# Kernel tuning notes

Measured on AMD Instinct MI355X. Metric: run time of the kernel, lower is better.

## Reference

```python
import jax, jax.numpy as jnp
import numpy as np

# ---- fixed architecture hyperparameters (match init_kwargs) ----
B, S = 4, 1024
L, H, DM, DF = 4, 8, 512, 2048
DH = DM // H          # 64 head dim (= 2*R after gated SPE filter)
NS = 5                # num_sines
R = 32                # num_realizations
M = 2 * DH            # favor_feature_dims = 128 (split as +/- of 64 projections)
LN_EPS = 1e-5
ATT_EPS = 1e-6


def layernorm(x, g, b):
    mu = x.mean(-1, keepdims=True)
    var = ((x - mu) ** 2).mean(-1, keepdims=True)
    return (x - mu) * jax.lax.rsqrt(var + LN_EPS) * g + b


def sine_spe(freqs, offsets, gains, noise, seq_len):
    """SineSPE positional code. freqs/offsets/gains: (H,DH,NS); noise: (H,DH,2NS,R).
    Returns qbar, kbar of shape (S,H,DH,R)."""
    pos = jnp.arange(seq_len, dtype=freqs.dtype)
    f = jax.nn.sigmoid(freqs)[:, :, None, :] / 2.0                       # (H,DH,1,NS)
    ph_q = 2.0 * jnp.pi * f * pos[None, None, :, None] + offsets[:, :, None, :]
    ph_k = 2.0 * jnp.pi * f * pos[None, None, :, None]
    om_q = jnp.stack([jnp.cos(ph_q), jnp.sin(ph_q)], -1).reshape(H, DH, seq_len, 2 * NS)
    om_k = jnp.stack([jnp.cos(ph_k), jnp.sin(ph_k)], -1).reshape(H, DH, seq_len, 2 * NS)
    g = jax.nn.softplus(gains)
    g = jnp.stack([g, g], -1).reshape(H, DH, 2 * NS)                      # upsample gains
    z = noise * g[..., None] / jnp.sqrt(jnp.asarray(2.0 * NS, freqs.dtype))
    qbar = jnp.einsum('hdsk,hdkr->shdr', om_q, z)
    kbar = jnp.einsum('hdsk,hdkr->shdr', om_k, z)
    scale = (R * DH) ** 0.25
    return qbar / scale, kbar / scale


def spe_filter(q, k, qbar, kbar, gate, gnoise):
    """Gated SPE filter. q,k: (B,S,H,DH); qbar/kbar: (S,H,DH,R); gate: (H,DH); gnoise: (H,DH,R).
    Returns qhat, khat of shape (B,S,H,2R)."""
    g = jax.nn.sigmoid(gate)[..., None]                                   # (H,DH,1)
    gn = gnoise / (DH * R) ** 0.25
    seq_len = qbar.shape[0]
    bias = jnp.broadcast_to(jnp.sqrt(g) * gn, (seq_len, H, DH, R))
    qb = jnp.concatenate([jnp.sqrt(1.0 - g) * qbar, bias], -1)            # (S,H,DH,2R)
    kb = jnp.concatenate([jnp.sqrt(1.0 - g) * kbar, bias], -1)
    qhat = jnp.einsum('bshd,shdr->bshr', q, qb)
    khat = jnp.einsum('bshd,shdr->bshr', k, kb)
    return qhat, khat


def favor(x, omega):
    """FAVOR+ softmax feature map. x: (B,S,H,DH); omega: (DH, M//2) -> (B,S,H,M)."""
    x = x * (DH ** -0.25)                                                 # sqrt(softmax_temp), temp=1/sqrt(DH)
    half_norm = 0.5 * jnp.sum(x * x, -1, keepdims=True)
    u = jnp.einsum('bshe,em->bshm', x, omega)
    phi = jnp.concatenate([jnp.exp(u - half_norm), jnp.exp(-u - half_norm)], -1)
    return phi / jnp.sqrt(jnp.asarray(M, x.dtype))


def causal_linear_attention(Q, K, V):
    """Causal linear (kernelized) attention via lax.scan. Q,K: (B,S,H,M); V: (B,S,H,DH)."""
    Bv = Q.shape[0]

    def step(carry, qkv):
        Skv, sk = carry
        q, k, v = qkv                                                     # (B,H,M),(B,H,M),(B,H,DH)
        Skv = Skv + jnp.einsum('bhm,bhd->bhmd', k, v)
        sk = sk + k
        num = jnp.einsum('bhm,bhmd->bhd', q, Skv)
        den = jnp.einsum('bhm,bhm->bh', q, sk) + ATT_EPS
        return (Skv, sk), num / den[..., None]

    init = (jnp.zeros((Bv, H, M, DH), Q.dtype), jnp.zeros((Bv, H, M), Q.dtype))
    xs = tuple(jnp.moveaxis(t, 1, 0) for t in (Q, K, V))
    _, out = jax.lax.scan(step, init, xs)
    return jnp.moveaxis(out, 0, 1)                                        # (B,S,H,DH)


def setup_inputs() -> dict:
    key = jax.random.key(0)
    ks = jax.random.split(key, 14)

    def rn(k, shape, scale=1.0):
        return jax.random.normal(k, shape, dtype=jnp.float32) * scale

    return {
        'x': rn(ks[0], (B, S, DM)),
        'Wq': rn(ks[1], (L, DM, DM), 0.02), 'bq': jnp.zeros((L, DM), jnp.float32),
        'Wk': rn(ks[2], (L, DM, DM), 0.02), 'bk': jnp.zeros((L, DM), jnp.float32),
        'Wv': rn(ks[3], (L, DM, DM), 0.02), 'bv': jnp.zeros((L, DM), jnp.float32),
        'Wo': rn(ks[4], (L, DM, DM), 0.02), 'bo': jnp.zeros((L, DM), jnp.float32),
        'W1': rn(ks[5], (L, DM, DF), 0.02), 'b1': jnp.zeros((L, DF), jnp.float32),
        'W2': rn(ks[6], (L, DF, DM), 0.02), 'b2': jnp.zeros((L, DM), jnp.float32),
        'ln1_g': jnp.ones((L, DM), jnp.float32), 'ln1_b': jnp.zeros((L, DM), jnp.float32),
        'ln2_g': jnp.ones((L, DM), jnp.float32), 'ln2_b': jnp.zeros((L, DM), jnp.float32),
        'spe_freqs': rn(ks[7], (L, H, DH, NS)),
        'spe_offsets': rn(ks[8], (L, H, DH, NS)),
        'spe_gains': rn(ks[9], (L, H, DH, NS)),
        'spe_noise': rn(ks[10], (L, H, DH, 2 * NS, R)),
        'gate': rn(ks[11], (L, H, DH)),
        'gate_noise': rn(ks[12], (L, H, DH, R)),
        'favor_omega': rn(ks[13], (L, DH, M // 2)),
    }


def reference(x, Wq, bq, Wk, bk, Wv, bv, Wo, bo, W1, b1, W2, b2,
              ln1_g, ln1_b, ln2_g, ln2_b,
              spe_freqs, spe_offsets, spe_gains, spe_noise, gate, gate_noise, favor_omega):
    Bv, Sv, _ = x.shape
    out = x
    for l in range(L):
        qbar, kbar = sine_spe(spe_freqs[l], spe_offsets[l], spe_gains[l], spe_noise[l], Sv)
        q = (out @ Wq[l] + bq[l]).reshape(Bv, Sv, H, DH)
        k = (out @ Wk[l] + bk[l]).reshape(Bv, Sv, H, DH)
        v = (out @ Wv[l] + bv[l]).reshape(Bv, Sv, H, DH)
        qh, kh = spe_filter(q, k, qbar, kbar, gate[l], gate_noise[l])
        Qf = favor(qh, favor_omega[l])
        Kf = favor(kh, favor_omega[l])
        att = causal_linear_attention(Qf, Kf, v).reshape(Bv, Sv, DM)
        att = att @ Wo[l] + bo[l]
        h = layernorm(out + att, ln1_g[l], ln1_b[l])
        y = jax.nn.relu(h @ W1[l] + b1[l]) @ W2[l] + b2[l]
        out = layernorm(h + y, ln2_g[l], ln2_b[l])
    return out
```

## Files before the change

kernel.cpp:

```cpp
#include <hip/hip_runtime.h>
#include <math.h>

#define BB 4
#define SS 1024
#define LL 4
#define HH 8
#define DM 512
#define DF 2048
#define DH 64
#define NS 5
#define RR 32
#define MM 128
#define NC 16
#define CHK 64
#define QKV_N 1536

#define INV_SQRT10   0.316227766016838f
#define INV_SCALE    0.148650889375340f
#define TEMP_SCALE   0.353553390593274f
#define INV_SQRT_M   0.088388347648318f
#define TWO_PI       6.283185307179586f
#define PI_F         3.141592653589793f

typedef __attribute__((ext_vector_type(8))) short bf16x8;
typedef __attribute__((ext_vector_type(4))) float f32x4;

__device__ __forceinline__ unsigned short f2bf(float f) {
  union { float f; unsigned int u; } v; v.f = f;
  unsigned int r = v.u + 0x7FFFu + ((v.u >> 16) & 1u);
  return (unsigned short)(r >> 16);
}

__device__ __forceinline__ float bf2f(unsigned short u) {
  union { unsigned int u; float f; } v; v.u = (unsigned int)u << 16;
  return v.f;
}

__device__ __forceinline__ void gld_lds16(const unsigned short* g, unsigned short* l) {
  __builtin_amdgcn_global_load_lds((const __attribute__((address_space(1))) void*)g,
                                   (__attribute__((address_space(3))) void*)l,
                                   16, 0, 0);
}

template<int RELU, int OUT_BF, int SPLITK>
__global__ __launch_bounds__(256)
void gemm_mfma_n64(const unsigned short* __restrict__ A, const unsigned short* __restrict__ Bt,
                   const float* __restrict__ bias, float* __restrict__ Cf,
                   unsigned short* __restrict__ Cbf, int M, int N, int K)
{
  __shared__ unsigned short As[128 * 32];
  __shared__ unsigned short Bs[64 * 32];
  const int tid  = threadIdx.x;
  const int w    = tid >> 6;
  const int lane = tid & 63;
  const int row0 = blockIdx.y * 128;
  const int col0 = blockIdx.x * 64;
  const int kz   = (SPLITK > 1) ? blockIdx.z : 0;
  const int Ks   = K / SPLITK;
  const int kbeg = kz * Ks;
  const int wr = (w >> 1) * 64;
  const int wc = (w & 1) * 32;
  const int c0 = w * 2, c1 = w * 2 + 1;
  const int m0 = c0 * 16 + (lane >> 2);
  const int m1 = c1 * 16 + (lane >> 2);
  const int mb = w * 16 + (lane >> 2);
  const int kA = (lane & 3) * 8;

  f32x4 acc[4][2] = {};

  for (int k0 = kbeg; k0 < kbeg + Ks; k0 += 32) {
    gld_lds16(&A [(size_t)(row0 + m0) * K + k0 + kA], &As[c0 * 512]);
    gld_lds16(&A [(size_t)(row0 + m1) * K + k0 + kA], &As[c1 * 512]);
    gld_lds16(&Bt[(size_t)(col0 + mb) * K + k0 + kA], &Bs[w * 512]);
    __syncthreads();
    const int rA = wr + (lane & 15);
    const int rB = wc + (lane & 15);
    const int kk = (lane >> 4) * 8;
    bf16x8 af[4], bfr[2];
#pragma unroll
    for (int i = 0; i < 4; ++i)
      af[i]  = *reinterpret_cast<const bf16x8*>(&As[(rA + i * 16) * 32 + kk]);
#pragma unroll
    for (int i = 0; i < 2; ++i)
      bfr[i] = *reinterpret_cast<const bf16x8*>(&Bs[(rB + i * 16) * 32 + kk]);
#pragma unroll
    for (int mi = 0; mi < 4; ++mi)
#pragma unroll
      for (int ni = 0; ni < 2; ++ni)
        acc[mi][ni] = __builtin_amdgcn_mfma_f32_16x16x32_bf16(af[mi], bfr[ni], acc[mi][ni], 0, 0, 0);
    __syncthreads();
  }
  const int cr = (lane >> 4) * 4;
  const int cc = lane & 15;
  float* Cfo = Cf ? (Cf + (size_t)kz * M * N) : Cf;
  unsigned short* Cbo = Cbf ? (Cbf + (size_t)kz * M * N) : Cbf;
#pragma unroll
  for (int mi = 0; mi < 4; ++mi) {
#pragma unroll
    for (int ni = 0; ni < 2; ++ni) {
      const int col = col0 + wc + ni * 16 + cc;
      const float bv = (kz == 0) ? bias[col] : 0.f;
#pragma unroll
      for (int r = 0; r < 4; ++r) {
        const int row = row0 + wr + mi * 16 + cr + r;
        float v = acc[mi][ni][r] + bv;
        if (RELU) v = fmaxf(v, 0.f);
        if (OUT_BF) Cbo[(size_t)row * N + col] = f2bf(v);
        else        Cfo[(size_t)row * N + col] = v;
      }
    }
  }
}

#define PR_T0   4096
#define PR_W1   8192
#define PR_W2   12288
#define PR_OM   12304
#define PR_PB   12328
#define PR_SP   15224
#define PR_CV   17272

__global__ __launch_bounds__(256)
void prep_all(const float* __restrict__ x,
              const float* __restrict__ Wq, const float* __restrict__ Wk,
              const float* __restrict__ Wv, const float* __restrict__ Wo,
              const float* __restrict__ W1, const float* __restrict__ W2,
              const float* __restrict__ omega,
              const float* __restrict__ bq, const float* __restrict__ bk,
              const float* __restrict__ bv,
              const float* __restrict__ gains, const float* __restrict__ noise,
              const float* __restrict__ gate, const float* __restrict__ gnoise,
              const float* __restrict__ offsets, const float* __restrict__ freqs,
              unsigned short* __restrict__ curbf,
              unsigned short* __restrict__ Wqkvt, unsigned short* __restrict__ Wot,
              unsigned short* __restrict__ W1t, unsigned short* __restrict__ W2t,
              unsigned short* __restrict__ omgT,
              float* __restrict__ bqkv,
              unsigned short* __restrict__ zpb, unsigned short* __restrict__ wbb,
              float2* __restrict__ offcs, float* __restrict__ omg)
{
  const int bid = blockIdx.x;
  const int tid = threadIdx.x;

  if (bid < PR_OM) {
    const float* W; unsigned short* Wt; int K, N, bx, by;
    if (bid < PR_T0) {
      const int mat = bid >> 10;
      const int local = bid & 1023;
      bx = local & 15; by = (local >> 4) & 15;
      const int l = local >> 8;
      K = DM; N = DM;
      if (mat == 0)      { W = Wq + (size_t)l * DM * DM; Wt = Wqkvt + (size_t)l * QKV_N * DM; }
      else if (mat == 1) { W = Wk + (size_t)l * DM * DM; Wt = Wqkvt + (size_t)l * QKV_N * DM + (size_t)512 * DM; }
      else if (mat == 2) { W = Wv + (size_t)l * DM * DM; Wt = Wqkvt + (size_t)l * QKV_N * DM + (size_t)1024 * DM; }
      else               { W = Wo + (size_t)l * DM * DM; Wt = Wot + (size_t)l * DM * DM; }
    } else if (bid < PR_W1) {
      const int local = bid - PR_T0;
      bx = local & 63; by = (local >> 6) & 15;
      const int l = local >> 10;
      K = DM; N = DF;
      W = W1 + (size_t)l * DM * DF; Wt = W1t + (size_t)l * DF * DM;
    } else if (bid < PR_W2) {
      const int local = bid - PR_W1;
      bx = local & 15; by = (local >> 4) & 63;
      const int l = local >> 10;
      K = DF; N = DM;
      W = W2 + (size_t)l * DF * DM; Wt = W2t + (size_t)l * DM * DF;
    } else {
      const int local = bid - PR_W2;
      bx = local & 1; by = (local >> 1) & 1;
      const int l = local >> 2;
      K = DH; N = MM / 2;
      W = omega + (size_t)l * DH * (MM / 2); Wt = omgT + (size_t)l * 4096;
    }
    __shared__ float tile[32][33];
    const int k0 = by * 32, n0 = bx * 32;
    const int tx = tid & 31, ty = tid >> 5;
#pragma unroll
    for (int j = 0; j < 4; ++j)
      tile[ty + 8 * j][tx] = W[(size_t)(k0 + ty + 8 * j) * N + n0 + tx];
    __syncthreads();
#pragma unroll
    for (int j = 0; j < 4; ++j)
      Wt[(size_t)(n0 + ty + 8 * j) * K + k0 + tx] = f2bf(tile[tx][ty + 8 * j]);
  } else if (bid < PR_PB) {
    const int local = bid - PR_OM;
    const int l = local / 6;
    const int i = (local % 6) * 256 + tid;
    if (i < QKV_N)
      bqkv[l * QKV_N + i] = (i < 512) ? bq[l * DM + i] : (i < 1024) ? bk[l * DM + i - 512]
                                                                    : bv[l * DM + i - 1024];
  } else if (bid < PR_SP) {
    const int i = (bid - PR_PB) * 256 + tid;
    const int NZ = LL * HH * RR * 10 * DH;
    const int NW = LL * HH * RR * DH;
    const int NO = LL * HH * DH * NS;
    if (i < NZ) {
      const int d = i & 63;
      int j = i >> 6;
      const int k = j % 10; j /= 10;
      const int r = j & 31; j >>= 5;
      const int h = j & 7;  const int l = j >> 3;
      const int lhd = (l * HH + h) * DH + d;
      const float ga = gains[lhd * NS + (k >> 1)];
      const float sp = (ga > 20.f) ? ga : log1pf(__expf(ga));
      const float gg = 1.f / (1.f + __expf(-gate[lhd]));
      const float c1 = sqrtf(fmaxf(1.f - gg, 0.f));
      const float nz = noise[((size_t)lhd * 10 + k) * 32 + r];
      zpb[i] = f2bf(nz * sp * c1 * (INV_SQRT10 * INV_SCALE * TEMP_SCALE));
    } else if (i < NZ + NW) {
      int j = i - NZ;
      const int d = j & 63; j >>= 6;
      const int r = j & 31; j >>= 5;
      const int h = j & 7;  const int l = j >> 3;
      const int lhd = (l * HH + h) * DH + d;
      const float gg = 1.f / (1.f + __expf(-gate[lhd]));
      wbb[i - NZ] = f2bf(sqrtf(gg) * gnoise[(size_t)lhd * 32 + r] * (INV_SCALE * TEMP_SCALE));
    } else if (i < NZ + NW + NO) {
      const int j = i - NZ - NW;
      float sn, cn;
      __sincosf(offsets[j], &sn, &cn);
      offcs[j] = make_float2(cn, sn);
    } else if (i < NZ + NW + 2 * NO) {
      const int j = i - NZ - NW - NO;
      omg[j] = PI_F / (1.f + __expf(-freqs[j]));
    }
  } else {
    const int i = (bid - PR_SP) * 256 + tid;
    const int n4 = BB * SS * DM / 4;
    if (i < n4) {
      const float4 v = reinterpret_cast<const float4*>(x)[i];
      ushort4 o;
      o.x = f2bf(v.x); o.y = f2bf(v.y); o.z = f2bf(v.z); o.w = f2bf(v.w);
      reinterpret_cast<ushort4*>(curbf)[i] = o;
    }
  }
}

__global__ __launch_bounds__(256)
void spe_xhat(const float* __restrict__ omg, const float2* __restrict__ offcs,
              const unsigned short* __restrict__ zpb, const unsigned short* __restrict__ wbb,
              const unsigned short* __restrict__ qkvb, const unsigned short* __restrict__ omgT,
              unsigned short* __restrict__ QfKfB)
{
  const int s = blockIdx.x;
  const int h = blockIdx.y;
  const int t = threadIdx.x;
  const int w = t >> 6;
  const int lane = t & 63;
  __shared__ float omqT[10][64];
  __shared__ float omkT[10][64];
  __shared__ unsigned short qbT[64 * 64];
  __shared__ unsigned short kbT[64 * 64];
  __shared__ unsigned short rQ[16 * 64];
  __shared__ unsigned short rK[16 * 64];
  __shared__ float hqp[4][8];
  __shared__ float hnl[8];

  for (int e = t; e < DH * NS; e += 256) {
    const int d = e / NS, ns = e - d * NS;
    const float om = omg[(h * DH + d) * NS + ns];
    float sn, cn;
    __sincosf(om * (float)s, &sn, &cn);
    const float2 oc = offcs[(h * DH + d) * NS + ns];
    omkT[2 * ns][d]     = cn;
    omkT[2 * ns + 1][d] = sn;
    omqT[2 * ns][d]     = cn * oc.x - sn * oc.y;
    omqT[2 * ns + 1][d] = sn * oc.x + cn * oc.y;
  }
  if (t < 64) {
    const int isK = t >> 5;
    const int b = (t >> 3) & 3;
    const int j = t & 7;
    const unsigned short* src = qkvb + ((size_t)b * SS + s) * QKV_N + isK * 512 + h * DH + j * 8;
    unsigned short* dst = (isK ? rK : rQ) + b * 64 + ((j ^ b) << 3);
    *reinterpret_cast<bf16x8*>(dst) = *reinterpret_cast<const bf16x8*>(src);
  } else if (t < 256) {
    const int i = t - 64;
    bf16x8 z = {};
    if (i < 96) *reinterpret_cast<bf16x8*>(&rQ[256 + i * 8]) = z;
    else        *reinterpret_cast<bf16x8*>(&rK[256 + (i - 96) * 8]) = z;
  }
  __syncthreads();
  {
    const int r = t >> 3, dg = t & 7, d0 = dg * 8;
    float accq[8] = {}, acck[8] = {};
    const unsigned short* zr = zpb + (size_t)(h * RR + r) * 10 * 64 + d0;
#pragma unroll
    for (int k = 0; k < 10; ++k) {
      const bf16x8 zv = *reinterpret_cast<const bf16x8*>(zr + (size_t)k * 64);
      const float4 oq0 = *reinterpret_cast<const float4*>(&omqT[k][d0]);
      const float4 oq1 = *reinterpret_cast<const float4*>(&omqT[k][d0 + 4]);
      const float4 ok0 = *reinterpret_cast<const float4*>(&omkT[k][d0]);
      const float4 ok1 = *reinterpret_cast<const float4*>(&omkT[k][d0 + 4]);
      float zf[8];
#pragma unroll
      for (int j = 0; j < 8; ++j) zf[j] = bf2f((unsigned short)zv[j]);
      accq[0] += zf[0] * oq0.x; accq[1] += zf[1] * oq0.y;
      accq[2] += zf[2] * oq0.z; accq[3] += zf[3] * oq0.w;
      accq[4] += zf[4] * oq1.x; accq[5] += zf[5] * oq1.y;
      accq[6] += zf[6] * oq1.z; accq[7] += zf[7] * oq1.w;
      acck[0] += zf[0] * ok0.x; acck[1] += zf[1] * ok0.y;
      acck[2] += zf[2] * ok0.z; acck[3] += zf[3] * ok0.w;
      acck[4] += zf[4] * ok1.x; acck[5] += zf[5] * ok1.y;
      acck[6] += zf[6] * ok1.z; acck[7] += zf[7] * ok1.w;
    }
    bf16x8 qv, kv;
#pragma unroll
    for (int j = 0; j < 8; ++j) {
      qv[j] = (short)f2bf(accq[j]);
      kv[j] = (short)f2bf(acck[j]);
    }
    const int sd0 = d0 ^ ((r & 7) << 3);
    *reinterpret_cast<bf16x8*>(&qbT[r * 64 + sd0]) = qv;
    *reinterpret_cast<bf16x8*>(&kbT[r * 64 + sd0]) = kv;
    const bf16x8 wv = *reinterpret_cast<const bf16x8*>(&wbb[(size_t)(h * RR + r) * 64 + d0]);
    *reinterpret_cast<bf16x8*>(&qbT[(32 + r) * 64 + sd0]) = wv;
    *reinterpret_cast<bf16x8*>(&kbT[(32 + r) * 64 + sd0]) = wv;
  }
  __syncthreads();
  f32x4 aq = {0.f, 0.f, 0.f, 0.f}, ak = {0.f, 0.f, 0.f, 0.f};
  const int arow = lane & 15;
  const int colr = w * 16 + (lane & 15);
#pragma unroll
  for (int kt = 0; kt < 2; ++kt) {
    const int g = kt * 4 + (lane >> 4);
    const bf16x8 fAq = *reinterpret_cast<const bf16x8*>(&rQ[arow * 64 + ((g ^ (arow & 7)) << 3)]);
    const bf16x8 fAk = *reinterpret_cast<const bf16x8*>(&rK[arow * 64 + ((g ^ (arow & 7)) << 3)]);
    const bf16x8 fBq = *reinterpret_cast<const bf16x8*>(&qbT[colr * 64 + ((g ^ (colr & 7)) << 3)]);
    const bf16x8 fBk = *reinterpret_cast<const bf16x8*>(&kbT[colr * 64 + ((g ^ (colr & 7)) << 3)]);
    aq = __builtin_amdgcn_mfma_f32_16x16x32_bf16(fAq, fBq, aq, 0, 0, 0);
    ak = __builtin_amdgcn_mfma_f32_16x16x32_bf16(fAk, fBk, ak, 0, 0, 0);
  }
  float rq[4], rk2[4];
#pragma unroll
  for (int r = 0; r < 4; ++r) { rq[r] = aq[r] * aq[r]; rk2[r] = ak[r] * ak[r]; }
#pragma unroll
  for (int off = 1; off < 16; off <<= 1) {
#pragma unroll
    for (int r = 0; r < 4; ++r) {
      rq[r]  += __shfl_xor(rq[r],  off, 64);
      rk2[r] += __shfl_xor(rk2[r], off, 64);
    }
  }
  if (lane == 0) {
#pragma unroll
    for (int r = 0; r < 4; ++r) { hqp[w][r] = rq[r]; hqp[w][4 + r] = rk2[r]; }
  }
  __syncthreads();

  if (t < 8) {
    const int b = t & 3;
    const int ko = (t >> 2) * 4;
    hnl[t] = 0.5f * (hqp[0][ko + b] + hqp[1][ko + b] + hqp[2][ko + b] + hqp[3][ko + b]);
  }
  if (lane < 16) {
#pragma unroll
    for (int r = 0; r < 4; ++r) {
      const int d = w * 16 + lane;
      rQ[r * 64 + (d ^ (r << 3))] = f2bf(aq[r]);
      rK[r * 64 + (d ^ (r << 3))] = f2bf(ak[r]);
    }
  }
  __syncthreads();

  f32x4 uq = {0.f, 0.f, 0.f, 0.f}, uk = {0.f, 0.f, 0.f, 0.f};
  const int ocol = w * 16 + (lane & 15);
#pragma unroll
  for (int kt = 0; kt < 2; ++kt) {
    const int g = kt * 4 + (lane >> 4);
    const bf16x8 fAq = *reinterpret_cast<const bf16x8*>(&rQ[arow * 64 + ((g ^ (arow & 7)) << 3)]);
    const bf16x8 fAk = *reinterpret_cast<const bf16x8*>(&rK[arow * 64 + ((g ^ (arow & 7)) << 3)]);
    const bf16x8 fB  = *reinterpret_cast<const bf16x8*>(&omgT[(size_t)ocol * 64 + g * 8]);
    uq = __builtin_amdgcn_mfma_f32_16x16x32_bf16(fAq, fB, uq, 0, 0, 0);
    uk = __builtin_amdgcn_mfma_f32_16x16x32_bf16(fAk, fB, uk, 0, 0, 0);
  }
  if (lane < 16) {
#pragma unroll
    for (int r = 0; r < 4; ++r) {
      const size_t rowq = ((size_t)r * SS + s) * HH + h;
      const size_t rowk = rowq + (size_t)BB * SS * HH;
      const float hq = hnl[r], hk = hnl[4 + r];
      QfKfB[rowq * MM + ocol]      = f2bf(__expf( uq[r] - hq) * INV_SQRT_M);
      QfKfB[rowq * MM + ocol + 64] = f2bf(__expf(-uq[r] - hq) * INV_SQRT_M);
      QfKfB[rowk * MM + ocol]      = f2bf(__expf( uk[r] - hk) * INV_SQRT_M);
      QfKfB[rowk * MM + ocol + 64] = f2bf(__expf(-uk[r] - hk) * INV_SQRT_M);
    }
  }
}

__global__ __launch_bounds__(256)
void attn_chunk_sums(const unsigned short* __restrict__ KfB, const unsigned short* __restrict__ qkvb,
                     unsigned short* __restrict__ SchB, float* __restrict__ kch)
{
  const int c = blockIdx.x, h = blockIdx.y, b = blockIdx.z;
  const int tid = threadIdx.x;
  const int w = tid >> 6, lane = tid & 63;
  __shared__ unsigned short KcT[128 * 64];
  __shared__ unsigned short VT[64 * 64];
  const size_t srow0 = (size_t)b * SS + c * CHK;

  for (int i = tid; i < 8192; i += 256) {
    const int m = i & 127, t = i >> 7;
    KcT[m * 64 + (t ^ ((m & 7) << 3))] = KfB[((srow0 + t) * HH + h) * MM + m];
  }
  for (int i = tid; i < 512; i += 256) {
    const int d = i & 63, oct = i >> 6;
    const unsigned short* src = qkvb + (srow0 + oct * 8) * QKV_N + 1024 + h * DH + d;
    bf16x8 v;
#pragma unroll
    for (int j = 0; j < 8; ++j) v[j] = (short)src[(size_t)j * QKV_N];
    *reinterpret_cast<bf16x8*>(&VT[d * 64 + ((oct << 3) ^ ((d & 7) << 3))]) = v;
  }
  __syncthreads();

  const int kk = (lane >> 4) * 8;
  f32x4 acc[2][4] = {};
#pragma unroll
  for (int kc = 0; kc < 2; ++kc) {
    const int k = kc * 32 + kk;
#pragma unroll
    for (int mi = 0; mi < 2; ++mi) {
      const int mA = w * 32 + mi * 16 + (lane & 15);
      const bf16x8 a = *reinterpret_cast<const bf16x8*>(&KcT[mA * 64 + (k ^ ((mA & 7) << 3))]);
#pragma unroll
      for (int ni = 0; ni < 4; ++ni) {
        const int dB = ni * 16 + (lane & 15);
        const bf16x8 bb = *reinterpret_cast<const bf16x8*>(&VT[dB * 64 + (k ^ ((dB & 7) << 3))]);
        acc[mi][ni] = __builtin_amdgcn_mfma_f32_16x16x32_bf16(a, bb, acc[mi][ni], 0, 0, 0);
      }
    }
  }
  const size_t base = (((size_t)b * HH + h) * NC + c);
  unsigned short* So = SchB + base * (MM * DH);
  const int cr = (lane >> 4) * 4, cc = lane & 15;
#pragma unroll
  for (int mi = 0; mi < 2; ++mi)
#pragma unroll
    for (int ni = 0; ni < 4; ++ni)
#pragma unroll
      for (int r = 0; r < 4; ++r)
        So[(size_t)(w * 32 + mi * 16 + cr + r) * DH + ni * 16 + cc] = f2bf(acc[mi][ni][r]);
  {
    const int m = tid >> 1, half = tid & 1;
    float ks = 0.f;
#pragma unroll
    for (int j = 0; j < 32; ++j) {
      const int t2 = half * 32 + j;
      ks += bf2f(KcT[m * 64 + (t2 ^ ((m & 7) << 3))]);
    }
    ks += __shfl_xor(ks, 1, 64);
    if (half == 0) kch[base * MM + m] = ks;
  }
}

__global__ __launch_bounds__(256)
void attn_scan(unsigned short* __restrict__ SchB, float* __restrict__ kch)
{
  const int bh = blockIdx.x, part = blockIdx.y;
  const int t = threadIdx.x;
  unsigned short* base = SchB + (size_t)bh * NC * (MM * DH);
  {
    const int e0 = part * 1024 + t * 4;
    float run0 = 0.f, run1 = 0.f, run2 = 0.f, run3 = 0.f;
#pragma unroll
    for (int c = 0; c < NC; ++c) {
      ushort4* p = reinterpret_cast<ushort4*>(&base[(size_t)c * (MM * DH) + e0]);
      const ushort4 v = *p;
      ushort4 o;
      o.x = f2bf(run0); o.y = f2bf(run1); o.z = f2bf(run2); o.w = f2bf(run3);
      *p = o;
      run0 += bf2f(v.x); run1 += bf2f(v.y); run2 += bf2f(v.z); run3 += bf2f(v.w);
    }
  }
  if (part == 0 && t < MM) {
    float* kb2 = kch + (size_t)bh * NC * MM;
    float run = 0.f;
#pragma unroll
    for (int c = 0; c < NC; ++c) {
      const float v = kb2[c * MM + t];
      kb2[c * MM + t] = run;
      run += v;
    }
  }
}

__global__ __launch_bounds__(256)
void attn_out(const unsigned short* __restrict__ QfKfB, const unsigned short* __restrict__ qkvb,
              const unsigned short* __restrict__ SchB, const float* __restrict__ kch,
              unsigned short* __restrict__ att)
{
  const int c = blockIdx.x, h = blockIdx.y, b = blockIdx.z;
  const int tid = threadIdx.x;
  const int w = tid >> 6;
  const int lane = tid & 63;
  __shared__ unsigned short Qc[64 * 128];
  __shared__ unsigned short Sb[64 * 64];
  __shared__ unsigned short KVU[12288];
  __shared__ float skp[MM];
  __shared__ float denl[64];

  unsigned short* Kc   = KVU;
  unsigned short* SpxT = KVU;
  unsigned short* VT   = KVU + 8192;

  const size_t srow0 = (size_t)b * SS + c * CHK;
  const unsigned short* Qg = QfKfB + (srow0 * HH + h) * MM;
  const unsigned short* Kg = Qg + (size_t)BB * SS * HH * MM;

  if (tid < MM) skp[tid] = kch[(((size_t)b * HH + h) * NC + c) * MM + tid];

  for (int i = tid; i < 1024; i += 256) {
    const int s2 = i >> 4, m8 = (i & 15) * 8;
    const int sw = m8 ^ ((s2 & 15) << 3);
    *reinterpret_cast<bf16x8*>(&Qc[s2 * 128 + sw]) =
        *reinterpret_cast<const bf16x8*>(&Qg[(size_t)s2 * (HH * MM) + m8]);
    *reinterpret_cast<bf16x8*>(&Kc[s2 * 128 + sw]) =
        *reinterpret_cast<const bf16x8*>(&Kg[(size_t)s2 * (HH * MM) + m8]);
  }
  for (int i = tid; i < 512; i += 256) {
    const int d = i & 63, oct = i >> 6;
    const unsigned short* src = qkvb + (srow0 + oct * 8) * QKV_N + 1024 + h * DH + d;
    bf16x8 v;
#pragma unroll
    for (int j = 0; j < 8; ++j) v[j] = (short)src[(size_t)j * QKV_N];
    *reinterpret_cast<bf16x8*>(&VT[d * 64 + ((oct << 3) ^ ((d & 7) << 3))]) = v;
  }
  __syncthreads();

  const int sA = w * 16 + (lane & 15);
  const int kk = (lane >> 4) * 8;
  f32x4 acc_s[4] = {};
#pragma unroll
  for (int kc = 0; kc < 4; ++kc) {
    const int k = kc * 32 + kk;
    const bf16x8 aq = *reinterpret_cast<const bf16x8*>(&Qc[sA * 128 + (k ^ ((sA & 15) << 3))]);
#pragma unroll
    for (int n = 0; n < 4; ++n) {
      const int tB = n * 16 + (lane & 15);
      const bf16x8 bq = *reinterpret_cast<const bf16x8*>(&Kc[tB * 128 + (k ^ ((tB & 15) << 3))]);
      acc_s[n] = __builtin_amdgcn_mfma_f32_16x16x32_bf16(aq, bq, acc_s[n], 0, 0, 0);
    }
  }
  __syncthreads();

  {
    const int g = lane >> 4;
    const int tcol = lane & 15;
    float dintra[4] = {0.f, 0.f, 0.f, 0.f};
#pragma unroll
    for (int r = 0; r < 4; ++r) {
      const int s = w * 16 + g * 4 + r;
#pragma unroll
      for (int n = 0; n < 4; ++n) {
        const int t2 = n * 16 + tcol;
        const float v = (t2 <= s) ? acc_s[n][r] : 0.f;
        dintra[r] += v;
        Sb[s * 64 + (t2 ^ ((s & 7) << 3))] = f2bf(v);
      }
    }
#pragma unroll
    for (int off = 1; off < 16; off <<= 1)
#pragma unroll
      for (int r = 0; r < 4; ++r) dintra[r] += __shfl_xor(dintra[r], off, 64);
    if (tcol == 0) {
#pragma unroll
      for (int r = 0; r < 4; ++r) denl[w * 16 + g * 4 + r] = dintra[r];
    }
  }
  {
    const unsigned short* Sp = SchB + (((size_t)b * HH + h) * NC + c) * (MM * DH);
    for (int i = tid; i < 1024; i += 256) {
      const int d = i & 63, oct = i >> 6;
      const unsigned short* src = Sp + (size_t)(oct * 8) * DH + d;
      bf16x8 v;
#pragma unroll
      for (int j = 0; j < 8; ++j) v[j] = (short)src[(size_t)j * DH];
      *reinterpret_cast<bf16x8*>(&SpxT[d * 128 + ((oct * 8) ^ ((d & 15) << 3))]) = v;
    }
  }
  __syncthreads();

  f32x4 acc_o[4] = {};
#pragma unroll
  for (int kc = 0; kc < 2; ++kc) {
    const int k = kc * 32 + kk;
    const bf16x8 as = *reinterpret_cast<const bf16x8*>(&Sb[sA * 64 + (k ^ ((sA & 7) << 3))]);
#pragma unroll
    for (int n = 0; n < 4; ++n) {
      const int dB = n * 16 + (lane & 15);
      const bf16x8 bv = *reinterpret_cast<const bf16x8*>(&VT[dB * 64 + (k ^ ((dB & 7) << 3))]);
      acc_o[n] = __builtin_amdgcn_mfma_f32_16x16x32_bf16(as, bv, acc_o[n], 0, 0, 0);
    }
  }
#pragma unroll
  for (int kc = 0; kc < 4; ++kc) {
    const int k = kc * 32 + kk;
    const bf16x8 aq = *reinterpret_cast<const bf16x8*>(&Qc[sA * 128 + (k ^ ((sA & 15) << 3))]);
#pragma unroll
    for (int n = 0; n < 4; ++n) {
      const int dB = n * 16 + (lane & 15);
      const bf16x8 bs = *reinterpret_cast<const bf16x8*>(&SpxT[dB * 128 + (k ^ ((dB & 15) << 3))]);
      acc_o[n] = __builtin_amdgcn_mfma_f32_16x16x32_bf16(aq, bs, acc_o[n], 0, 0, 0);
    }
  }
  {
    const int s2 = tid >> 2, part = tid & 3;
    float p = 0.f;
#pragma unroll
    for (int j = 0; j < 32; ++j) {
      const int m = part * 32 + j;
      p += bf2f(Qc[s2 * 128 + (m ^ ((s2 & 15) << 3))]) * skp[m];
    }
    p += __shfl_xor(p, 1, 64);
    p += __shfl_xor(p, 2, 64);
    if (part == 0) denl[s2] += p + 1e-6f;
  }
  __syncthreads();

  {
    const int g = lane >> 4;
    const int dcol = lane & 15;
#pragma unroll
    for (int r = 0; r < 4; ++r) {
      const int s = w * 16 + g * 4 + r;
      const float dinv = 1.f / denl[s];
#pragma unroll
      for (int n = 0; n < 4; ++n)
        att[(srow0 + s) * DM + h * DH + n * 16 + dcol] = f2bf(acc_o[n][r] * dinv);
    }
  }
}

template<int WBF>
__global__ __launch_bounds__(256)
void add_ln(const float* __restrict__ a, const unsigned short* __restrict__ bres, size_t sstride,
            const float* __restrict__ g, const float* __restrict__ be,
            float* __restrict__ out, unsigned short* __restrict__ outbf)
{
  const int row = blockIdx.x;
  const int t = threadIdx.x;
  const size_t base = (size_t)row * DM;
  float x0 = a[base + t]       + bf2f(bres[base + t])       + bf2f(bres[sstride + base + t]);
  float x1 = a[base + t + 256] + bf2f(bres[base + t + 256]) + bf2f(bres[sstride + base + t + 256]);
  __shared__ float red[8];
  float ssum = x0 + x1;
#pragma unroll
  for (int off = 32; off > 0; off >>= 1) ssum += __shfl_xor(ssum, off, 64);
  const int wid = t >> 6, lid = t & 63;
  if (lid == 0) red[wid] = ssum;
  __syncthreads();
  const float mu = (red[0] + red[1] + red[2] + red[3]) * (1.f / DM);
  const float d0 = x0 - mu, d1 = x1 - mu;
  float sv = d0 * d0 + d1 * d1;
#pragma unroll
  for (int off = 32; off > 0; off >>= 1) sv += __shfl_xor(sv, off, 64);
  if (lid == 0) red[4 + wid] = sv;
  __syncthreads();
  const float var = (red[4] + red[5] + red[6] + red[7]) * (1.f / DM);
  const float rs = rsqrtf(var + 1e-5f);
  const float o0 = d0 * rs * g[t]       + be[t];
  const float o1 = d1 * rs * g[t + 256] + be[t + 256];
  out[base + t]       = o0;
  out[base + t + 256] = o1;
  if (WBF) {
    outbf[base + t]       = f2bf(o0);
    outbf[base + t + 256] = f2bf(o1);
  }
}

extern "C" void kernel_launch(void* const* d_in, const int* in_sizes, int n_in,
                              void* d_out, int out_size, void* d_ws, size_t ws_size,
                              hipStream_t stream)
{
  const float* x      = (const float*)d_in[0];
  const float* Wq     = (const float*)d_in[1];
  const float* bq     = (const float*)d_in[2];
  const float* Wk     = (const float*)d_in[3];
  const float* bk     = (const float*)d_in[4];
  const float* Wv     = (const float*)d_in[5];
  const float* bv     = (const float*)d_in[6];
  const float* Wo     = (const float*)d_in[7];
  const float* bo     = (const float*)d_in[8];
  const float* W1     = (const float*)d_in[9];
  const float* b1     = (const float*)d_in[10];
  const float* W2     = (const float*)d_in[11];
  const float* b2     = (const float*)d_in[12];
  const float* ln1g   = (const float*)d_in[13];
  const float* ln1b   = (const float*)d_in[14];
  const float* ln2g   = (const float*)d_in[15];
  const float* ln2b   = (const float*)d_in[16];
  const float* freqs  = (const float*)d_in[17];
  const float* offs   = (const float*)d_in[18];
  const float* gains  = (const float*)d_in[19];
  const float* noise  = (const float*)d_in[20];
  const float* gate   = (const float*)d_in[21];
  const float* gnoise = (const float*)d_in[22];
  const float* omega  = (const float*)d_in[23];

  float* ws = (float*)d_ws;
  size_t o = 0;
  float* curf = ws + o; o += (size_t)BB * SS * DM;
  unsigned short* qkvb = (unsigned short*)(ws + o); o += (size_t)BB * SS * QKV_N / 2;
  float* Sch  = ws + o; o += (size_t)BB * HH * NC * MM * DH;
  float* kch  = ws + o; o += (size_t)BB * HH * NC * MM;
  float* bqkv = ws + o; o += (size_t)LL * QKV_N;
  float2* offcs = (float2*)(ws + o); o += (size_t)LL * HH * DH * NS * 2;
  float* omgf = ws + o; o += (size_t)LL * HH * DH * NS;
  unsigned short* zpb = (unsigned short*)(ws + o); o += (size_t)LL * HH * RR * 10 * DH / 2;
  unsigned short* QfKfB = (unsigned short*)(ws + o); o += (size_t)2 * BB * SS * HH * MM / 2;
  unsigned short* attb  = (unsigned short*)(ws + o); o += (size_t)BB * SS * DM / 2;
  unsigned short* h_bf  = (unsigned short*)(ws + o); o += (size_t)BB * SS * DM / 2;
  unsigned short* curbf = (unsigned short*)(ws + o); o += (size_t)BB * SS * DM / 2;
  unsigned short* Wqkvt = (unsigned short*)(ws + o); o += (size_t)LL * QKV_N * DM / 2;
  unsigned short* Wot   = (unsigned short*)(ws + o); o += (size_t)LL * DM * DM / 2;
  unsigned short* W1t   = (unsigned short*)(ws + o); o += (size_t)LL * DF * DM / 2;
  unsigned short* W2t   = (unsigned short*)(ws + o); o += (size_t)LL * DM * DF / 2;
  unsigned short* omgT  = (unsigned short*)(ws + o); o += (size_t)LL * 4096 / 2;
  unsigned short* wbb   = (unsigned short*)(ws + o); o += (size_t)LL * HH * RR * DH / 2;

  const size_t SLICE = (size_t)BB * SS * DM;
  unsigned short* SchB  = (unsigned short*)Sch;
  unsigned short* attpB = (unsigned short*)Sch;
  unsigned short* ybufB = (unsigned short*)Sch;
  float* hbuf = (float*)qkvb;
  unsigned short* midbf = QfKfB;
  unsigned short* KfB   = QfKfB + (size_t)BB * SS * HH * MM;

  const int MROWS = BB * SS;

  prep_all<<<PR_CV, 256, 0, stream>>>(x, Wq, Wk, Wv, Wo, W1, W2, omega,
                                      bq, bk, bv, gains, noise, gate, gnoise, offs, freqs,
                                      curbf, Wqkvt, Wot, W1t, W2t, omgT, bqkv,
                                      zpb, wbb, offcs, omgf);

  for (int l = 0; l < LL; ++l) {
    const float* in = (l == 0) ? x : curf;

    gemm_mfma_n64<0, 1, 1><<<dim3(QKV_N / 64, MROWS / 128), 256, 0, stream>>>(
        curbf, Wqkvt + (size_t)l * QKV_N * DM, bqkv + (size_t)l * QKV_N,
        (float*)nullptr, qkvb, MROWS, QKV_N, DM);

    spe_xhat<<<dim3(SS, HH), 256, 0, stream>>>(
        omgf + (size_t)l * HH * DH * NS, offcs + (size_t)l * HH * DH * NS,
        zpb + (size_t)l * HH * RR * 10 * DH, wbb + (size_t)l * HH * RR * DH,
        qkvb, omgT + (size_t)l * 4096, QfKfB);

    attn_chunk_sums<<<dim3(NC, HH, BB), 256, 0, stream>>>(KfB, qkvb, SchB, kch);
    attn_scan<<<dim3(BB * HH, 8), 256, 0, stream>>>(SchB, kch);
    attn_out<<<dim3(NC, HH, BB), 256, 0, stream>>>(QfKfB, qkvb, SchB, kch, attb);

    gemm_mfma_n64<0, 1, 2><<<dim3(DM / 64, MROWS / 128, 2), 256, 0, stream>>>(
        attb, Wot + (size_t)l * DM * DM, bo + (size_t)l * DM,
        (float*)nullptr, attpB, MROWS, DM, DM);

    add_ln<1><<<MROWS, 256, 0, stream>>>(in, attpB, SLICE,
        ln1g + (size_t)l * DM, ln1b + (size_t)l * DM, hbuf, h_bf);

    gemm_mfma_n64<1, 1, 1><<<dim3(DF / 64, MROWS / 128), 256, 0, stream>>>(
        h_bf, W1t + (size_t)l * DF * DM, b1 + (size_t)l * DF, (float*)nullptr, midbf, MROWS, DF, DM);

    gemm_mfma_n64<0, 1, 2><<<dim3(DM / 64, MROWS / 128, 2), 256, 0, stream>>>(
        midbf, W2t + (size_t)l * DM * DF, b2 + (size_t)l * DM,
        (float*)nullptr, ybufB, MROWS, DM, DF);

    if (l == LL - 1) {
      add_ln<0><<<MROWS, 256, 0, stream>>>(hbuf, ybufB, SLICE,
          ln2g + (size_t)l * DM, ln2b + (size_t)l * DM, (float*)d_out, (unsigned short*)nullptr);
    } else {
      add_ln<1><<<MROWS, 256, 0, stream>>>(hbuf, ybufB, SLICE,
          ln2g + (size_t)l * DM, ln2b + (size_t)l * DM, curf, curbf);
    }
  }
}
```

Before: 629.6 us.

## Restructure SPE filter as direct K=640 MFMA contraction over noise

Rather than materialising the per-position qbar/kbar filter matrices in shared memory through a scalar FMA loop and then multiplying by q/k, the kernel now forms y = q ⊙ omega in shared memory. It contracts y against the precomputed noise matrix with a single K=640 MFMA chain, plus a separate small MFMA for the gate-noise bias half. Each wave now handles one side (Q or K) and one 16-column tile instead of both sides, and rows 4-15 of the MFMA A operand are zero-filled in registers. The goal is to remove the scalar filter-build loop and the shared-memory staging it needed. In exchange, more MFMA instructions are issued on mostly-padded rows, the noise operand is read straight from global memory, and rounding changes because y is cast to bf16 before the contraction.

```diff
diff --git a/kernel.cpp b/kernel.cpp
--- a/kernel.cpp
+++ b/kernel.cpp
@@ -250,11 +250,11 @@
   const int lane = t & 63;
   __shared__ float omqT[10][64];
   __shared__ float omkT[10][64];
-  __shared__ unsigned short qbT[64 * 64];
-  __shared__ unsigned short kbT[64 * 64];
-  __shared__ unsigned short rQ[16 * 64];
-  __shared__ unsigned short rK[16 * 64];
-  __shared__ float hqp[4][8];
+  __shared__ unsigned short yQ[4 * 640];
+  __shared__ unsigned short yK[4 * 640];
+  __shared__ unsigned short rQ[4 * 64];
+  __shared__ unsigned short rK[4 * 64];
+  __shared__ float hqp[4][4];
   __shared__ float hnl[8];
 
   for (int e = t; e < DH * NS; e += 256) {
@@ -275,91 +275,84 @@
     const unsigned short* src = qkvb + ((size_t)b * SS + s) * QKV_N + isK * 512 + h * DH + j * 8;
     unsigned short* dst = (isK ? rK : rQ) + b * 64 + ((j ^ b) << 3);
     *reinterpret_cast<bf16x8*>(dst) = *reinterpret_cast<const bf16x8*>(src);
-  } else if (t < 256) {
-    const int i = t - 64;
-    bf16x8 z = {};
-    if (i < 96) *reinterpret_cast<bf16x8*>(&rQ[256 + i * 8]) = z;
-    else        *reinterpret_cast<bf16x8*>(&rK[256 + (i - 96) * 8]) = z;
-  }
-  __syncthreads();
-  {
-    const int r = t >> 3, dg = t & 7, d0 = dg * 8;
-    float accq[8] = {}, acck[8] = {};
-    const unsigned short* zr = zpb + (size_t)(h * RR + r) * 10 * 64 + d0;
-#pragma unroll
-    for (int k = 0; k < 10; ++k) {
-      const bf16x8 zv = *reinterpret_cast<const bf16x8*>(zr + (size_t)k * 64);
-      const float4 oq0 = *reinterpret_cast<const float4*>(&omqT[k][d0]);
-      const float4 oq1 = *reinterpret_cast<const float4*>(&omqT[k][d0 + 4]);
-      const float4 ok0 = *reinterpret_cast<const float4*>(&omkT[k][d0]);
-      const float4 ok1 = *reinterpret_cast<const float4*>(&omkT[k][d0 + 4]);
-      float zf[8];
-#pragma unroll
-      for (int j = 0; j < 8; ++j) zf[j] = bf2f((unsigned short)zv[j]);
-      accq[0] += zf[0] * oq0.x; accq[1] += zf[1] * oq0.y;
-      accq[2] += zf[2] * oq0.z; accq[3] += zf[3] * oq0.w;
-      accq[4] += zf[4] * oq1.x; accq[5] += zf[5] * oq1.y;
-      accq[6] += zf[6] * oq1.z; accq[7] += zf[7] * oq1.w;
-      acck[0] += zf[0] * ok0.x; acck[1] += zf[1] * ok0.y;
-      acck[2] += zf[2] * ok0.z; acck[3] += zf[3] * ok0.w;
-      acck[4] += zf[4] * ok1.x; acck[5] += zf[5] * ok1.y;
-      acck[6] += zf[6] * ok1.z; acck[7] += zf[7] * ok1.w;
-    }
-    bf16x8 qv, kv;
-#pragma unroll
-    for (int j = 0; j < 8; ++j) {
-      qv[j] = (short)f2bf(accq[j]);
-      kv[j] = (short)f2bf(acck[j]);
-    }
-    const int sd0 = d0 ^ ((r & 7) << 3);
-    *reinterpret_cast<bf16x8*>(&qbT[r * 64 + sd0]) = qv;
-    *reinterpret_cast<bf16x8*>(&kbT[r * 64 + sd0]) = kv;
-    const bf16x8 wv = *reinterpret_cast<const bf16x8*>(&wbb[(size_t)(h * RR + r) * 64 + d0]);
-    *reinterpret_cast<bf16x8*>(&qbT[(32 + r) * 64 + sd0]) = wv;
-    *reinterpret_cast<bf16x8*>(&kbT[(32 + r) * 64 + sd0]) = wv;
-  }
-  __syncthreads();
-  f32x4 aq = {0.f, 0.f, 0.f, 0.f}, ak = {0.f, 0.f, 0.f, 0.f};
+  }
+  __syncthreads();
+
+  for (int i = t; i < 640; i += 256) {
+    const int sidei = (i >= 320) ? 1 : 0;
+    const int o2 = i - sidei * 320;
+    const int b = o2 / 80;
+    const int oct = o2 - b * 80;
+    const int k = oct >> 3;
+    const int d0 = (oct & 7) * 8;
+    const unsigned short* src = qkvb + ((size_t)b * SS + s) * QKV_N + sidei * 512 + h * DH + d0;
+    const bf16x8 qv = *reinterpret_cast<const bf16x8*>(src);
+    const float* omp = sidei ? &omkT[k][d0] : &omqT[k][d0];
+    bf16x8 yv;
+#pragma unroll
+    for (int j = 0; j < 8; ++j)
+      yv[j] = (short)f2bf(bf2f((unsigned short)qv[j]) * omp[j]);
+    unsigned short* dst = (sidei ? yK : yQ) + b * 640 + ((oct ^ b) << 3);
+    *reinterpret_cast<bf16x8*>(dst) = yv;
+  }
+  __syncthreads();
+
+  const int side = w >> 1;
+  const int nt   = w & 1;
   const int arow = lane & 15;
-  const int colr = w * 16 + (lane & 15);
+  const int g    = lane >> 4;
+  const unsigned short* yA  = side ? yK : yQ;
+  const unsigned short* rA_ = side ? rK : rQ;
+  const unsigned short* zh  = zpb + (size_t)h * RR * 640;
+  const unsigned short* wh  = wbb + (size_t)h * RR * 64;
+  const int rB = nt * 16 + (lane & 15);
+  const bf16x8 zerov = {};
+
+  f32x4 acc1 = {0.f, 0.f, 0.f, 0.f};
+  f32x4 acc2 = {0.f, 0.f, 0.f, 0.f};
+#pragma unroll
+  for (int kt = 0; kt < 20; ++kt) {
+    const int oct = kt * 4 + g;
+    bf16x8 fA = zerov;
+    if (arow < 4) fA = *reinterpret_cast<const bf16x8*>(&yA[arow * 640 + ((oct ^ arow) << 3)]);
+    const bf16x8 fB = *reinterpret_cast<const bf16x8*>(&zh[(size_t)rB * 640 + kt * 32 + g * 8]);
+    acc1 = __builtin_amdgcn_mfma_f32_16x16x32_bf16(fA, fB, acc1, 0, 0, 0);
+  }
 #pragma unroll
   for (int kt = 0; kt < 2; ++kt) {
-    const int g = kt * 4 + (lane >> 4);
-    const bf16x8 fAq = *reinterpret_cast<const bf16x8*>(&rQ[arow * 64 + ((g ^ (arow & 7)) << 3)]);
-    const bf16x8 fAk = *reinterpret_cast<const bf16x8*>(&rK[arow * 64 + ((g ^ (arow & 7)) << 3)]);
-    const bf16x8 fBq = *reinterpret_cast<const bf16x8*>(&qbT[colr * 64 + ((g ^ (colr & 7)) << 3)]);
-    const bf16x8 fBk = *reinterpret_cast<const bf16x8*>(&kbT[colr * 64 + ((g ^ (colr & 7)) << 3)]);
-    aq = __builtin_amdgcn_mfma_f32_16x16x32_bf16(fAq, fBq, aq, 0, 0, 0);
-    ak = __builtin_amdgcn_mfma_f32_16x16x32_bf16(fAk, fBk, ak, 0, 0, 0);
-  }
-  float rq[4], rk2[4];
-#pragma unroll
-  for (int r = 0; r < 4; ++r) { rq[r] = aq[r] * aq[r]; rk2[r] = ak[r] * ak[r]; }
-#pragma unroll
-  for (int off = 1; off < 16; off <<= 1) {
-#pragma unroll
-    for (int r = 0; r < 4; ++r) {
-      rq[r]  += __shfl_xor(rq[r],  off, 64);
-      rk2[r] += __shfl_xor(rk2[r], off, 64);
-    }
-  }
+    const int oct = kt * 4 + g;
+    bf16x8 fA = zerov;
+    if (arow < 4) fA = *reinterpret_cast<const bf16x8*>(&rA_[arow * 64 + ((oct ^ arow) << 3)]);
+    const bf16x8 fB = *reinterpret_cast<const bf16x8*>(&wh[(size_t)rB * 64 + kt * 32 + g * 8]);
+    acc2 = __builtin_amdgcn_mfma_f32_16x16x32_bf16(fA, fB, acc2, 0, 0, 0);
+  }
+
+  float rq[4];
+#pragma unroll
+  for (int r = 0; r < 4; ++r) rq[r] = acc1[r] * acc1[r] + acc2[r] * acc2[r];
+#pragma unroll
+  for (int off = 1; off < 16; off <<= 1)
+#pragma unroll
+    for (int r = 0; r < 4; ++r) rq[r] += __shfl_xor(rq[r], off, 64);
   if (lane == 0) {
 #pragma unroll
-    for (int r = 0; r < 4; ++r) { hqp[w][r] = rq[r]; hqp[w][4 + r] = rk2[r]; }
+    for (int r = 0; r < 4; ++r) hqp[w][r] = rq[r];
   }
   __syncthreads();
 
   if (t < 8) {
     const int b = t & 3;
-    const int ko = (t >> 2) * 4;
-    hnl[t] = 0.5f * (hqp[0][ko + b] + hqp[1][ko + b] + hqp[2][ko + b] + hqp[3][ko + b]);
+    const int sd = t >> 2;
+    hnl[t] = 0.5f * (hqp[sd * 2][b] + hqp[sd * 2 + 1][b]);
   }
   if (lane < 16) {
+    unsigned short* dst = side ? rK : rQ;
 #pragma unroll
     for (int r = 0; r < 4; ++r) {
-      const int d = w * 16 + lane;
-      rQ[r * 64 + (d ^ (r << 3))] = f2bf(aq[r]);
-      rK[r * 64 + (d ^ (r << 3))] = f2bf(ak[r]);
+      const int c1 = nt * 16 + lane;
+      const int c2 = 32 + nt * 16 + lane;
+      dst[r * 64 + (c1 ^ (r << 3))] = f2bf(acc1[r]);
+      dst[r * 64 + (c2 ^ (r << 3))] = f2bf(acc2[r]);
     }
   }
   __syncthreads();
@@ -368,10 +361,13 @@
   const int ocol = w * 16 + (lane & 15);
 #pragma unroll
   for (int kt = 0; kt < 2; ++kt) {
-    const int g = kt * 4 + (lane >> 4);
-    const bf16x8 fAq = *reinterpret_cast<const bf16x8*>(&rQ[arow * 64 + ((g ^ (arow & 7)) << 3)]);
-    const bf16x8 fAk = *reinterpret_cast<const bf16x8*>(&rK[arow * 64 + ((g ^ (arow & 7)) << 3)]);
-    const bf16x8 fB  = *reinterpret_cast<const bf16x8*>(&omgT[(size_t)ocol * 64 + g * 8]);
+    const int oct = kt * 4 + g;
+    bf16x8 fAq = zerov, fAk = zerov;
+    if (arow < 4) {
+      fAq = *reinterpret_cast<const bf16x8*>(&rQ[arow * 64 + ((oct ^ arow) << 3)]);
+      fAk = *reinterpret_cast<const bf16x8*>(&rK[arow * 64 + ((oct ^ arow) << 3)]);
+    }
+    const bf16x8 fB = *reinterpret_cast<const bf16x8*>(&omgT[(size_t)ocol * 64 + oct * 8]);
     uq = __builtin_amdgcn_mfma_f32_16x16x32_bf16(fAq, fB, uq, 0, 0, 0);
     uk = __builtin_amdgcn_mfma_f32_16x16x32_bf16(fAk, fB, uk, 0, 0, 0);
   }
```

Result: slower. 827.1 us (+31.4%).

## Widen GEMM tiles to 128x128 and spread SPE feature writes across all lanes

Applied to the files above, without the earlier changes.

The bf16 MFMA GEMM moves from 128x64 to 128x128 output tiles. Each wave now computes a 64x64 sub-tile with 16 accumulators, which doubles the work done per A-tile load and halves the number of blocks. The spe_xhat epilogue now uses shuffles so that all 64 lanes write one row each, instead of only 16 lanes looping over 4 rows. The larger tiles reduce grid parallelism (the Wo and W2 GEMMs drop to 64 blocks with split-K) and raise register pressure.

```diff
diff --git a/kernel.cpp b/kernel.cpp
--- a/kernel.cpp
+++ b/kernel.cpp
@@ -44,49 +44,48 @@
 
 template<int RELU, int OUT_BF, int SPLITK>
 __global__ __launch_bounds__(256)
-void gemm_mfma_n64(const unsigned short* __restrict__ A, const unsigned short* __restrict__ Bt,
+void gemm_mfma_128(const unsigned short* __restrict__ A, const unsigned short* __restrict__ Bt,
                    const float* __restrict__ bias, float* __restrict__ Cf,
                    unsigned short* __restrict__ Cbf, int M, int N, int K)
 {
   __shared__ unsigned short As[128 * 32];
-  __shared__ unsigned short Bs[64 * 32];
+  __shared__ unsigned short Bs[128 * 32];
   const int tid  = threadIdx.x;
   const int w    = tid >> 6;
   const int lane = tid & 63;
   const int row0 = blockIdx.y * 128;
-  const int col0 = blockIdx.x * 64;
+  const int col0 = blockIdx.x * 128;
   const int kz   = (SPLITK > 1) ? blockIdx.z : 0;
   const int Ks   = K / SPLITK;
   const int kbeg = kz * Ks;
   const int wr = (w >> 1) * 64;
-  const int wc = (w & 1) * 32;
+  const int wc = (w & 1) * 64;
   const int c0 = w * 2, c1 = w * 2 + 1;
   const int m0 = c0 * 16 + (lane >> 2);
   const int m1 = c1 * 16 + (lane >> 2);
-  const int mb = w * 16 + (lane >> 2);
   const int kA = (lane & 3) * 8;
 
-  f32x4 acc[4][2] = {};
+  f32x4 acc[4][4] = {};
 
   for (int k0 = kbeg; k0 < kbeg + Ks; k0 += 32) {
     gld_lds16(&A [(size_t)(row0 + m0) * K + k0 + kA], &As[c0 * 512]);
     gld_lds16(&A [(size_t)(row0 + m1) * K + k0 + kA], &As[c1 * 512]);
-    gld_lds16(&Bt[(size_t)(col0 + mb) * K + k0 + kA], &Bs[w * 512]);
+    gld_lds16(&Bt[(size_t)(col0 + m0) * K + k0 + kA], &Bs[c0 * 512]);
+    gld_lds16(&Bt[(size_t)(col0 + m1) * K + k0 + kA], &Bs[c1 * 512]);
     __syncthreads();
     const int rA = wr + (lane & 15);
     const int rB = wc + (lane & 15);
     const int kk = (lane >> 4) * 8;
-    bf16x8 af[4], bfr[2];
-#pragma unroll
-    for (int i = 0; i < 4; ++i)
+    bf16x8 af[4], bfr[4];
+#pragma unroll
+    for (int i = 0; i < 4; ++i) {
       af[i]  = *reinterpret_cast<const bf16x8*>(&As[(rA + i * 16) * 32 + kk]);
-#pragma unroll
-    for (int i = 0; i < 2; ++i)
       bfr[i] = *reinterpret_cast<const bf16x8*>(&Bs[(rB + i * 16) * 32 + kk]);
+    }
 #pragma unroll
     for (int mi = 0; mi < 4; ++mi)
 #pragma unroll
-      for (int ni = 0; ni < 2; ++ni)
+      for (int ni = 0; ni < 4; ++ni)
         acc[mi][ni] = __builtin_amdgcn_mfma_f32_16x16x32_bf16(af[mi], bfr[ni], acc[mi][ni], 0, 0, 0);
     __syncthreads();
   }
@@ -97,7 +96,7 @@
 #pragma unroll
   for (int mi = 0; mi < 4; ++mi) {
 #pragma unroll
-    for (int ni = 0; ni < 2; ++ni) {
+    for (int ni = 0; ni < 4; ++ni) {
       const int col = col0 + wc + ni * 16 + cc;
       const float bv = (kz == 0) ? bias[col] : 0.f;
 #pragma unroll
@@ -354,13 +353,17 @@
     const int ko = (t >> 2) * 4;
     hnl[t] = 0.5f * (hqp[0][ko + b] + hqp[1][ko + b] + hqp[2][ko + b] + hqp[3][ko + b]);
   }
-  if (lane < 16) {
-#pragma unroll
-    for (int r = 0; r < 4; ++r) {
-      const int d = w * 16 + lane;
-      rQ[r * 64 + (d ^ (r << 3))] = f2bf(aq[r]);
-      rK[r * 64 + (d ^ (r << 3))] = f2bf(ak[r]);
-    }
+  {
+    const int rr = lane >> 4, cc2 = lane & 15;
+    const float a0 = __shfl(aq[0], cc2, 64), a1 = __shfl(aq[1], cc2, 64);
+    const float a2 = __shfl(aq[2], cc2, 64), a3 = __shfl(aq[3], cc2, 64);
+    const float b0 = __shfl(ak[0], cc2, 64), b1 = __shfl(ak[1], cc2, 64);
+    const float b2 = __shfl(ak[2], cc2, 64), b3 = __shfl(ak[3], cc2, 64);
+    const float va = rr == 0 ? a0 : rr == 1 ? a1 : rr == 2 ? a2 : a3;
+    const float vb = rr == 0 ? b0 : rr == 1 ? b1 : rr == 2 ? b2 : b3;
+    const int d = w * 16 + cc2;
+    rQ[rr * 64 + (d ^ (rr << 3))] = f2bf(va);
+    rK[rr * 64 + (d ^ (rr << 3))] = f2bf(vb);
   }
   __syncthreads();
 
@@ -375,17 +378,22 @@
     uq = __builtin_amdgcn_mfma_f32_16x16x32_bf16(fAq, fB, uq, 0, 0, 0);
     uk = __builtin_amdgcn_mfma_f32_16x16x32_bf16(fAk, fB, uk, 0, 0, 0);
   }
-  if (lane < 16) {
-#pragma unroll
-    for (int r = 0; r < 4; ++r) {
-      const size_t rowq = ((size_t)r * SS + s) * HH + h;
-      const size_t rowk = rowq + (size_t)BB * SS * HH;
-      const float hq = hnl[r], hk = hnl[4 + r];
-      QfKfB[rowq * MM + ocol]      = f2bf(__expf( uq[r] - hq) * INV_SQRT_M);
-      QfKfB[rowq * MM + ocol + 64] = f2bf(__expf(-uq[r] - hq) * INV_SQRT_M);
-      QfKfB[rowk * MM + ocol]      = f2bf(__expf( uk[r] - hk) * INV_SQRT_M);
-      QfKfB[rowk * MM + ocol + 64] = f2bf(__expf(-uk[r] - hk) * INV_SQRT_M);
-    }
+  {
+    const int rr = lane >> 4, cc2 = lane & 15;
+    const float q0 = __shfl(uq[0], cc2, 64), q1 = __shfl(uq[1], cc2, 64);
+    const float q2 = __shfl(uq[2], cc2, 64), q3 = __shfl(uq[3], cc2, 64);
+    const float k0 = __shfl(uk[0], cc2, 64), k1 = __shfl(uk[1], cc2, 64);
+    const float k2 = __shfl(uk[2], cc2, 64), k3 = __shfl(uk[3], cc2, 64);
+    const float vq = rr == 0 ? q0 : rr == 1 ? q1 : rr == 2 ? q2 : q3;
+    const float vk = rr == 0 ? k0 : rr == 1 ? k1 : rr == 2 ? k2 : k3;
+    const float hq = hnl[rr], hk = hnl[4 + rr];
+    const size_t rowq = ((size_t)rr * SS + s) * HH + h;
+    const size_t rowk = rowq + (size_t)BB * SS * HH;
+    const int oc = w * 16 + cc2;
+    QfKfB[rowq * MM + oc]      = f2bf(__expf( vq - hq) * INV_SQRT_M);
+    QfKfB[rowq * MM + oc + 64] = f2bf(__expf(-vq - hq) * INV_SQRT_M);
+    QfKfB[rowk * MM + oc]      = f2bf(__expf( vk - hk) * INV_SQRT_M);
+    QfKfB[rowk * MM + oc + 64] = f2bf(__expf(-vk - hk) * INV_SQRT_M);
   }
 }
 
@@ -737,7 +745,7 @@
   for (int l = 0; l < LL; ++l) {
     const float* in = (l == 0) ? x : curf;
 
-    gemm_mfma_n64<0, 1, 1><<<dim3(QKV_N / 64, MROWS / 128), 256, 0, stream>>>(
+    gemm_mfma_128<0, 1, 1><<<dim3(QKV_N / 128, MROWS / 128), 256, 0, stream>>>(
         curbf, Wqkvt + (size_t)l * QKV_N * DM, bqkv + (size_t)l * QKV_N,
         (float*)nullptr, qkvb, MROWS, QKV_N, DM);
 
@@ -750,17 +758,17 @@
     attn_scan<<<dim3(BB * HH, 8), 256, 0, stream>>>(SchB, kch);
     attn_out<<<dim3(NC, HH, BB), 256, 0, stream>>>(QfKfB, qkvb, SchB, kch, attb);
 
-    gemm_mfma_n64<0, 1, 2><<<dim3(DM / 64, MROWS / 128, 2), 256, 0, stream>>>(
+    gemm_mfma_128<0, 1, 2><<<dim3(DM / 128, MROWS / 128, 2), 256, 0, stream>>>(
         attb, Wot + (size_t)l * DM * DM, bo + (size_t)l * DM,
         (float*)nullptr, attpB, MROWS, DM, DM);
 
     add_ln<1><<<MROWS, 256, 0, stream>>>(in, attpB, SLICE,
         ln1g + (size_t)l * DM, ln1b + (size_t)l * DM, hbuf, h_bf);
 
-    gemm_mfma_n64<1, 1, 1><<<dim3(DF / 64, MROWS / 128), 256, 0, stream>>>(
+    gemm_mfma_128<1, 1, 1><<<dim3(DF / 128, MROWS / 128), 256, 0, stream>>>(
         h_bf, W1t + (size_t)l * DF * DM, b1 + (size_t)l * DF, (float*)nullptr, midbf, MROWS, DF, DM);
 
-    gemm_mfma_n64<0, 1, 2><<<dim3(DM / 64, MROWS / 128, 2), 256, 0, stream>>>(
+    gemm_mfma_128<0, 1, 2><<<dim3(DM / 128, MROWS / 128, 2), 256, 0, stream>>>(
         midbf, W2t + (size_t)l * DM * DF, b2 + (size_t)l * DM,
         (float*)nullptr, ybufB, MROWS, DM, DF);
 
```

Measured after the change: 665.0 us. 5.6% more time.
